# Performance work log

Measured on AMD Instinct MI355X. Metric: run time of the kernel, lower is better.

## Reference

```python
import jax, jax.numpy as jnp
import numpy as np

# Winograd F(4x4, 3x3) transform matrices (m=4, r=3, a=6)
B_T = jnp.array([[4.,0.,-5.,0.,1.,0.],
                 [0.,-4.,-4.,1.,1.,0.],
                 [0.,4.,-4.,-1.,1.,0.],
                 [0.,-2.,-1.,2.,1.,0.],
                 [0.,2.,-1.,-2.,1.,0.],
                 [0.,4.,0.,-5.,0.,1.]], dtype=jnp.float32)
G = jnp.array([[1/4.,0.,0.],
               [-1/6.,-1/6.,-1/6.],
               [-1/6.,1/6.,-1/6.],
               [1/24.,1/12.,1/6.],
               [1/24.,-1/12.,1/6.],
               [0.,0.,1.]], dtype=jnp.float32)
A_T = jnp.array([[1.,1.,1.,1.,1.,0.],
                 [0.,1.,-1.,2.,-2.,0.],
                 [0.,1.,1.,4.,4.,0.],
                 [0.,1.,-1.,8.,-8.,1.]], dtype=jnp.float32)

M_OUT, R_K, A_IN = 4, 3, 6  # output tile m, kernel r, input tile a = m+r-1


def setup_inputs() -> dict:
    key = jax.random.key(0)
    k1, k2 = jax.random.split(key)
    x = jax.random.normal(k1, (16, 64, 130, 130), dtype=jnp.float32)
    w = jax.random.normal(k2, (64, 64, 3, 3), dtype=jnp.float32) * 0.05
    return {"input": x, "weight": w}


def reference(input, weight):
    N, C, H, W = input.shape
    K = weight.shape[0]
    m, r, a = M_OUT, R_K, A_IN
    T = (H - r + 1) // m  # tiles per spatial dim (perfect tiling)

    # Filter transform: U[k,c] = G @ w[k,c] @ G^T  -> [K,C,a,a]
    U = jnp.einsum('ai,kcij,bj->kcab', G, weight, G)

    # Extract overlapping a x a input tiles with stride m: [N,C,T,a,T,a]
    idx = (jnp.arange(T) * m)[:, None] + jnp.arange(a)[None, :]  # [T,a]
    tiles = input[:, :, idx, :][:, :, :, :, idx]

    # Input transform: V = B^T @ tile @ B  -> [N,T,T,C,a,a]
    V = jnp.einsum('ai,nctisj,bj->ntscab', B_T, tiles, B_T)
    Vp = V.reshape(N * T * T, C, a, a)  # [P,C,a,a]

    # Elementwise (tile-domain) multiply + channel reduce: M[p,k] = sum_c U[k,c]*V[p,c]
    Mt = jnp.einsum('kcab,pcab->pkab', U, Vp)  # [P,K,a,a]

    # Output transform: Y_tile = A^T @ M @ A -> [P,K,m,m]
    Yt = jnp.einsum('ai,pkij,bj->pkab', A_T, Mt, A_T)

    out = T * m  # = H - r + 1
    Y = Yt.reshape(N, T, T, K, m, m).transpose(0, 3, 1, 4, 2, 5).reshape(N, K, out, out)
    return Y
```

## Files before the change

### kernel.cpp

```cpp
#include <hip/hip_runtime.h>


__constant__ float c_AT[24] = {
  1.f, 0.f, 0.f, 0.f,
  1.f, 1.f, 1.f, 1.f,
  1.f,-1.f, 1.f,-1.f,
  1.f, 2.f, 4.f, 8.f,
  1.f,-2.f, 4.f,-8.f,
  0.f, 0.f, 0.f, 1.f
};

__device__ __forceinline__ void gl2lds16(const float* g, float* l) {
  __builtin_amdgcn_global_load_lds((const __attribute__((address_space(1))) void*)g,
                                   (__attribute__((address_space(3))) void*)l, 16, 0, 0);
}

__global__ __launch_bounds__(256) void k_filter(const float* __restrict__ w,
                                                float* __restrict__ U) {
  int g = blockIdx.x * 256 + threadIdx.x;
  int k = g & 63;
  int c = g >> 6;
  const float* wp = w + (size_t)(k * 64 + c) * 9;
  float w00 = wp[0], w01 = wp[1], w02 = wp[2];
  float w10 = wp[3], w11 = wp[4], w12 = wp[5];
  float w20 = wp[6], w21 = wp[7], w22 = wp[8];
  const float G[6][3] = {
    {0.25f, 0.f, 0.f},
    {-1.f/6.f, -1.f/6.f, -1.f/6.f},
    {-1.f/6.f,  1.f/6.f, -1.f/6.f},
    {1.f/24.f,  1.f/12.f, 1.f/6.f},
    {1.f/24.f, -1.f/12.f, 1.f/6.f},
    {0.f, 0.f, 1.f}
  };
  float t[6][3];
#pragma unroll
  for (int a = 0; a < 6; ++a) {
    t[a][0] = G[a][0]*w00 + G[a][1]*w10 + G[a][2]*w20;
    t[a][1] = G[a][0]*w01 + G[a][1]*w11 + G[a][2]*w21;
    t[a][2] = G[a][0]*w02 + G[a][1]*w12 + G[a][2]*w22;
  }
#pragma unroll
  for (int a = 0; a < 6; ++a) {
#pragma unroll
    for (int b = 0; b < 6; ++b) {
      float u = G[b][0]*t[a][0] + G[b][1]*t[a][1] + G[b][2]*t[a][2];
      U[(size_t)(a*6+b)*4096 + c*64 + k] = u;
    }
  }
}

__global__ __launch_bounds__(256) void k_input(const float* __restrict__ x,
                                               float* __restrict__ V,
                                               int n0, int Pchunk) {
  __shared__ float Ls[34*134];
  const int tid  = threadIdx.x;
  const int bi   = blockIdx.x;
  const int band = bi & 3;
  const int c    = (bi >> 2) & 63;
  const int nl   = bi >> 8;
  const float* xp = x + (size_t)((n0 + nl) * 64 + c) * (130*130) + band * 32 * 130;
  for (int idx = tid; idx < 34*65; idx += 256) {
    int r  = idx / 65;
    int c2 = idx - r * 65;
    *(float2*)&Ls[r*134 + c2*2] = *(const float2*)(xp + r*130 + c2*2);
  }
  __syncthreads();
  const int tyl = tid >> 5;
  const int tx  = tid & 31;
  const int ty  = band * 8 + tyl;
  const int p   = (nl * 32 + ty) * 32 + tx;
  const float* bl = &Ls[(tyl*4)*134 + tx*4];
  float t1[6][6];
#pragma unroll
  for (int j = 0; j < 6; ++j) {
    float d0 = bl[0*134+j], d1 = bl[1*134+j], d2 = bl[2*134+j];
    float d3 = bl[3*134+j], d4 = bl[4*134+j], d5 = bl[5*134+j];
    t1[0][j] =  4.f*d0 - 5.f*d2 + d4;
    t1[1][j] = -4.f*d1 - 4.f*d2 + d3 + d4;
    t1[2][j] =  4.f*d1 - 4.f*d2 - d3 + d4;
    t1[3][j] = -2.f*d1 -     d2 + 2.f*d3 + d4;
    t1[4][j] =  2.f*d1 -     d2 - 2.f*d3 + d4;
    t1[5][j] =  4.f*d1 - 5.f*d3 + d5;
  }
  float* vb = V + (size_t)c * Pchunk + p;
  const size_t abs_ = (size_t)64 * Pchunk;
#pragma unroll
  for (int a = 0; a < 6; ++a) {
    float s0=t1[a][0], s1=t1[a][1], s2=t1[a][2], s3=t1[a][3], s4=t1[a][4], s5=t1[a][5];
    float v0 =  4.f*s0 - 5.f*s2 + s4;
    float v1 = -4.f*s1 - 4.f*s2 + s3 + s4;
    float v2 =  4.f*s1 - 4.f*s2 - s3 + s4;
    float v3 = -2.f*s1 -     s2 + 2.f*s3 + s4;
    float v4 =  2.f*s1 -     s2 - 2.f*s3 + s4;
    float v5 =  4.f*s1 - 5.f*s3 + s5;
    vb[(size_t)(a*6+0)*abs_] = v0;
    vb[(size_t)(a*6+1)*abs_] = v1;
    vb[(size_t)(a*6+2)*abs_] = v2;
    vb[(size_t)(a*6+3)*abs_] = v3;
    vb[(size_t)(a*6+4)*abs_] = v4;
    vb[(size_t)(a*6+5)*abs_] = v5;
  }
}

__global__ __launch_bounds__(256) void k_gemm2(const float* __restrict__ V,
                                               const float* __restrict__ U,
                                               float* __restrict__ M,
                                               int Pchunk, int nPB) {
  __shared__ float Vs[64*256];
  __shared__ float Us[64*64];
  const int tid  = threadIdx.x;
  const int lane = tid & 63;
  const int wv   = tid >> 6;
  const unsigned bx = blockIdx.x;
  const int ab = bx / (unsigned)nPB;
  const int pb = bx - ab * nPB;
  const int p0 = pb * 256;

  const float* Vab = V + (size_t)ab * 64 * Pchunk + p0;
  const float* Uab = U + (size_t)ab * 4096;

#pragma unroll
  for (int i = 0; i < 16; ++i) {
    int r = wv + i * 4;
    gl2lds16(Vab + (size_t)r * Pchunk + lane * 4, &Vs[r * 256]);
  }
#pragma unroll
  for (int i = 0; i < 4; ++i) {
    int li = wv + i * 4;
    gl2lds16(Uab + li * 256 + lane * 4, &Us[li * 256]);
  }
  __syncthreads();

  const int pt = tid & 31;
  const int kt = tid >> 5;
  float acc[8][8];
#pragma unroll
  for (int ki = 0; ki < 8; ++ki)
#pragma unroll
    for (int pi = 0; pi < 8; ++pi) acc[ki][pi] = 0.f;

#pragma unroll 4
  for (int c = 0; c < 64; ++c) {
    const float4 va = *(const float4*)&Vs[c*256 + pt*4];
    const float4 vb = *(const float4*)&Vs[c*256 + 128 + pt*4];
    const float4 ua = *(const float4*)&Us[c*64 + kt*8];
    const float4 ub = *(const float4*)&Us[c*64 + kt*8 + 4];
    const float vv[8] = {va.x, va.y, va.z, va.w, vb.x, vb.y, vb.z, vb.w};
    const float uu[8] = {ua.x, ua.y, ua.z, ua.w, ub.x, ub.y, ub.z, ub.w};
#pragma unroll
    for (int ki = 0; ki < 8; ++ki)
#pragma unroll
      for (int pi = 0; pi < 8; ++pi)
        acc[ki][pi] += uu[ki] * vv[pi];
  }

#pragma unroll
  for (int ki = 0; ki < 8; ++ki) {
    float* mb = M + ((size_t)ab * 64 + kt*8 + ki) * Pchunk + p0;
    *(float4*)(mb + pt*4)       = make_float4(acc[ki][0], acc[ki][1], acc[ki][2], acc[ki][3]);
    *(float4*)(mb + 128 + pt*4) = make_float4(acc[ki][4], acc[ki][5], acc[ki][6], acc[ki][7]);
  }
}

__global__ __launch_bounds__(256) void k_out(const float* __restrict__ M,
                                             float* __restrict__ out,
                                             int n0, int Pchunk, int bpk) {
  const unsigned bx = blockIdx.x;
  const int k    = bx / (unsigned)bpk;
  const int pblk = bx - k * bpk;
  const int p    = pblk * 256 + threadIdx.x;
  const int nl = p >> 10;
  const int ty = (p >> 5) & 31;
  const int tx = p & 31;

  const float* mp = M + (size_t)k * Pchunk + p;
  const size_t abstride = (size_t)64 * Pchunk;
  float m[36];
#pragma unroll
  for (int ab = 0; ab < 36; ++ab) m[ab] = mp[(size_t)ab * abstride];

  float Y[4][4];
#pragma unroll
  for (int u = 0; u < 4; ++u)
#pragma unroll
    for (int v = 0; v < 4; ++v) Y[u][v] = 0.f;

#pragma unroll
  for (int i = 0; i < 6; ++i) {
    float R[4] = {0.f, 0.f, 0.f, 0.f};
#pragma unroll
    for (int j = 0; j < 6; ++j) {
      float mm = m[i*6 + j];
#pragma unroll
      for (int v = 0; v < 4; ++v) R[v] += c_AT[j*4 + v] * mm;
    }
#pragma unroll
    for (int u = 0; u < 4; ++u) {
      float au = c_AT[i*4 + u];
#pragma unroll
      for (int v = 0; v < 4; ++v) Y[u][v] += au * R[v];
    }
  }

  float* ob = out + ((size_t)((n0 + nl) * 64 + k) * 128 + ty*4) * 128 + tx*4;
#pragma unroll
  for (int u = 0; u < 4; ++u)
    *(float4*)(ob + (size_t)u * 128) = make_float4(Y[u][0], Y[u][1], Y[u][2], Y[u][3]);
}

extern "C" void kernel_launch(void* const* d_in, const int* in_sizes, int n_in,
                              void* d_out, int out_size, void* d_ws, size_t ws_size,
                              hipStream_t stream) {
  const float* x = (const float*)d_in[0];
  const float* w = (const float*)d_in[1];
  float* out = (float*)d_out;
  float* U = (float*)d_ws;
  const size_t U_bytes = 36ull * 64 * 64 * 4;
  const size_t per_n = 2ull * 36 * 1024 * 64 * 4;
  size_t avail = ws_size > U_bytes ? ws_size - U_bytes : 0;
  int chunk = (int)(avail / per_n);
  if (chunk < 1) return;
  if (chunk > 16) chunk = 16;

  k_filter<<<16, 256, 0, stream>>>(w, U);
  for (int n0 = 0; n0 < 16; n0 += chunk) {
    int cn = (16 - n0) < chunk ? (16 - n0) : chunk;
    int Pchunk = cn * 1024;
    float* V = (float*)((char*)d_ws + U_bytes);
    float* M = V + (size_t)36 * 64 * Pchunk;
    int nPB = cn * 4;
    k_input<<<cn*256,  256, 0, stream>>>(x, V, n0, Pchunk);
    k_gemm2<<<36*nPB,  256, 0, stream>>>(V, U, M, Pchunk, nPB);
    k_out  <<<64*nPB,  256, 0, stream>>>(M, out, n0, Pchunk, nPB);
  }
}
```

Measured before the change: 268.6 us.

## Double-buffer GEMM channel stages, widen output-transform tiles, halve batch chunk

The tile-domain GEMM now processes 512 tile positions per block. It loads V in 16-channel double-buffered LDS stages so global loads overlap compute, and reads U through wave-uniform scalar loads instead of LDS, with each wave owning 16 output channels. The output transform handles four adjacent tiles per thread, using float4 loads of M and 16-float contiguous row stores. The batch chunk is capped at 8, so the pipeline runs in two passes with a smaller V/M working set that may stay cache-resident, at the cost of extra launches and higher register pressure in the GEMM.

```diff
diff --git a/kernel.cpp b/kernel.cpp
--- a/kernel.cpp
+++ b/kernel.cpp
@@ -102,110 +102,127 @@
   }
 }
 
-__global__ __launch_bounds__(256) void k_gemm2(const float* __restrict__ V,
-                                               const float* __restrict__ U,
-                                               float* __restrict__ M,
-                                               int Pchunk, int nPB) {
-  __shared__ float Vs[64*256];
-  __shared__ float Us[64*64];
+__global__ __launch_bounds__(256, 2) void k_gemm3(const float* __restrict__ V,
+                                                  const float* __restrict__ U,
+                                                  float* __restrict__ M,
+                                                  int Pchunk, int nPB) {
+  __shared__ float Vs[2][16][512];
   const int tid  = threadIdx.x;
   const int lane = tid & 63;
   const int wv   = tid >> 6;
   const unsigned bx = blockIdx.x;
   const int ab = bx / (unsigned)nPB;
   const int pb = bx - ab * nPB;
-  const int p0 = pb * 256;
-
+  const int p0 = pb * 512;
   const float* Vab = V + (size_t)ab * 64 * Pchunk + p0;
   const float* Uab = U + (size_t)ab * 4096;
-
-#pragma unroll
-  for (int i = 0; i < 16; ++i) {
-    int r = wv + i * 4;
-    gl2lds16(Vab + (size_t)r * Pchunk + lane * 4, &Vs[r * 256]);
-  }
-#pragma unroll
-  for (int i = 0; i < 4; ++i) {
-    int li = wv + i * 4;
-    gl2lds16(Uab + li * 256 + lane * 4, &Us[li * 256]);
-  }
-  __syncthreads();
-
-  const int pt = tid & 31;
-  const int kt = tid >> 5;
-  float acc[8][8];
-#pragma unroll
-  for (int ki = 0; ki < 8; ++ki)
-#pragma unroll
-    for (int pi = 0; pi < 8; ++pi) acc[ki][pi] = 0.f;
-
-#pragma unroll 4
-  for (int c = 0; c < 64; ++c) {
-    const float4 va = *(const float4*)&Vs[c*256 + pt*4];
-    const float4 vb = *(const float4*)&Vs[c*256 + 128 + pt*4];
-    const float4 ua = *(const float4*)&Us[c*64 + kt*8];
-    const float4 ub = *(const float4*)&Us[c*64 + kt*8 + 4];
-    const float vv[8] = {va.x, va.y, va.z, va.w, vb.x, vb.y, vb.z, vb.w};
-    const float uu[8] = {ua.x, ua.y, ua.z, ua.w, ub.x, ub.y, ub.z, ub.w};
-#pragma unroll
-    for (int ki = 0; ki < 8; ++ki)
-#pragma unroll
-      for (int pi = 0; pi < 8; ++pi)
-        acc[ki][pi] += uu[ki] * vv[pi];
-  }
-
-#pragma unroll
-  for (int ki = 0; ki < 8; ++ki) {
-    float* mb = M + ((size_t)ab * 64 + kt*8 + ki) * Pchunk + p0;
-    *(float4*)(mb + pt*4)       = make_float4(acc[ki][0], acc[ki][1], acc[ki][2], acc[ki][3]);
-    *(float4*)(mb + 128 + pt*4) = make_float4(acc[ki][4], acc[ki][5], acc[ki][6], acc[ki][7]);
-  }
-}
-
-__global__ __launch_bounds__(256) void k_out(const float* __restrict__ M,
-                                             float* __restrict__ out,
-                                             int n0, int Pchunk, int bpk) {
+  const int k0 = __builtin_amdgcn_readfirstlane(wv * 16);
+
+#define STAGE(cc, buf)                                                        \
+  {                                                                           \
+    _Pragma("unroll")                                                         \
+    for (int i = 0; i < 8; ++i) {                                             \
+      int h = wv * 8 + i;                                                     \
+      int r = h >> 1, hf = h & 1;                                             \
+      gl2lds16(Vab + (size_t)((cc)*16 + r) * Pchunk + hf*256 + lane*4,        \
+               &Vs[(buf)][r][hf*256]);                                        \
+    }                                                                         \
+  }
+
+  float acc[16][8];
+#pragma unroll
+  for (int kk = 0; kk < 16; ++kk)
+#pragma unroll
+    for (int pp = 0; pp < 8; ++pp) acc[kk][pp] = 0.f;
+
+  STAGE(0, 0);
+  for (int cc = 0; cc < 4; ++cc) {
+    __syncthreads();
+    if (cc < 3) STAGE(cc + 1, (cc + 1) & 1);
+    const float* vsb = &Vs[cc & 1][0][0];
+#pragma unroll
+    for (int c = 0; c < 16; ++c) {
+      const float* uc = Uab + (size_t)(cc * 16 + c) * 64 + k0;
+      float4 va = *(const float4*)(vsb + c * 512 + lane * 4);
+      float4 vb = *(const float4*)(vsb + c * 512 + 256 + lane * 4);
+      float vv[8] = {va.x, va.y, va.z, va.w, vb.x, vb.y, vb.z, vb.w};
+#pragma unroll
+      for (int kk = 0; kk < 16; ++kk) {
+        float u = uc[kk];
+#pragma unroll
+        for (int pp = 0; pp < 8; ++pp) acc[kk][pp] += u * vv[pp];
+      }
+    }
+  }
+#undef STAGE
+
+  float* mb = M + ((size_t)ab * 64 + k0) * Pchunk + p0;
+#pragma unroll
+  for (int kk = 0; kk < 16; ++kk) {
+    *(float4*)(mb + (size_t)kk * Pchunk + lane * 4) =
+        make_float4(acc[kk][0], acc[kk][1], acc[kk][2], acc[kk][3]);
+    *(float4*)(mb + (size_t)kk * Pchunk + 256 + lane * 4) =
+        make_float4(acc[kk][4], acc[kk][5], acc[kk][6], acc[kk][7]);
+  }
+}
+
+__global__ __launch_bounds__(256) void k_out2(const float* __restrict__ M,
+                                              float* __restrict__ out,
+                                              int n0, int Pchunk, int bpk) {
   const unsigned bx = blockIdx.x;
   const int k    = bx / (unsigned)bpk;
   const int pblk = bx - k * bpk;
-  const int p    = pblk * 256 + threadIdx.x;
+  const int p    = pblk * 1024 + threadIdx.x * 4;
   const int nl = p >> 10;
   const int ty = (p >> 5) & 31;
   const int tx = p & 31;
 
   const float* mp = M + (size_t)k * Pchunk + p;
   const size_t abstride = (size_t)64 * Pchunk;
-  float m[36];
-#pragma unroll
-  for (int ab = 0; ab < 36; ++ab) m[ab] = mp[(size_t)ab * abstride];
-
-  float Y[4][4];
+
+  float Y[4][4][4];
 #pragma unroll
   for (int u = 0; u < 4; ++u)
 #pragma unroll
-    for (int v = 0; v < 4; ++v) Y[u][v] = 0.f;
+    for (int v = 0; v < 4; ++v)
+#pragma unroll
+      for (int q = 0; q < 4; ++q) Y[u][v][q] = 0.f;
 
 #pragma unroll
   for (int i = 0; i < 6; ++i) {
-    float R[4] = {0.f, 0.f, 0.f, 0.f};
+    float R[4][4];
+#pragma unroll
+    for (int v = 0; v < 4; ++v)
+#pragma unroll
+      for (int q = 0; q < 4; ++q) R[v][q] = 0.f;
 #pragma unroll
     for (int j = 0; j < 6; ++j) {
-      float mm = m[i*6 + j];
-#pragma unroll
-      for (int v = 0; v < 4; ++v) R[v] += c_AT[j*4 + v] * mm;
+      float4 m4 = *(const float4*)(mp + (size_t)(i * 6 + j) * abstride);
+      float mm[4] = {m4.x, m4.y, m4.z, m4.w};
+#pragma unroll
+      for (int v = 0; v < 4; ++v) {
+        float av = c_AT[j * 4 + v];
+#pragma unroll
+        for (int q = 0; q < 4; ++q) R[v][q] += av * mm[q];
+      }
     }
 #pragma unroll
     for (int u = 0; u < 4; ++u) {
-      float au = c_AT[i*4 + u];
-#pragma unroll
-      for (int v = 0; v < 4; ++v) Y[u][v] += au * R[v];
-    }
-  }
-
-  float* ob = out + ((size_t)((n0 + nl) * 64 + k) * 128 + ty*4) * 128 + tx*4;
+      float au = c_AT[i * 4 + u];
+#pragma unroll
+      for (int v = 0; v < 4; ++v)
+#pragma unroll
+        for (int q = 0; q < 4; ++q) Y[u][v][q] += au * R[v][q];
+    }
+  }
+
+  float* ob = out + ((size_t)((n0 + nl) * 64 + k) * 128 + ty * 4) * 128 + tx * 4;
 #pragma unroll
   for (int u = 0; u < 4; ++u)
-    *(float4*)(ob + (size_t)u * 128) = make_float4(Y[u][0], Y[u][1], Y[u][2], Y[u][3]);
+    *(float4*)(ob + (size_t)u * 128) = make_float4(Y[u][0][0], Y[u][1][0], Y[u][2][0], Y[u][3][0])
+    , *(float4*)(ob + (size_t)u * 128 + 4)  = make_float4(Y[u][0][1], Y[u][1][1], Y[u][2][1], Y[u][3][1])
+    , *(float4*)(ob + (size_t)u * 128 + 8)  = make_float4(Y[u][0][2], Y[u][1][2], Y[u][2][2], Y[u][3][2])
+    , *(float4*)(ob + (size_t)u * 128 + 12) = make_float4(Y[u][0][3], Y[u][1][3], Y[u][2][3], Y[u][3][3]);
 }
 
 extern "C" void kernel_launch(void* const* d_in, const int* in_sizes, int n_in,
@@ -220,7 +237,7 @@
   size_t avail = ws_size > U_bytes ? ws_size - U_bytes : 0;
   int chunk = (int)(avail / per_n);
   if (chunk < 1) return;
-  if (chunk > 16) chunk = 16;
+  if (chunk > 8) chunk = 8;
 
   k_filter<<<16, 256, 0, stream>>>(w, U);
   for (int n0 = 0; n0 < 16; n0 += chunk) {
@@ -228,9 +245,9 @@
     int Pchunk = cn * 1024;
     float* V = (float*)((char*)d_ws + U_bytes);
     float* M = V + (size_t)36 * 64 * Pchunk;
-    int nPB = cn * 4;
-    k_input<<<cn*256,  256, 0, stream>>>(x, V, n0, Pchunk);
-    k_gemm2<<<36*nPB,  256, 0, stream>>>(V, U, M, Pchunk, nPB);
-    k_out  <<<64*nPB,  256, 0, stream>>>(M, out, n0, Pchunk, nPB);
-  }
-}
+    int nPBg = cn * 2;
+    k_input<<<cn*256,   256, 0, stream>>>(x, V, n0, Pchunk);
+    k_gemm3<<<36*nPBg,  256, 0, stream>>>(V, U, M, Pchunk, nPBg);
+    k_out2 <<<64*cn,    256, 0, stream>>>(M, out, n0, Pchunk, cn);
+  }
+}
```

Result: slower. 298.4 us (+11.1%).
